# Kernel tuning notes

Measured on AMD Instinct MI355X. Metric: run time of the kernel, lower is better.

Reference implementation:

```python
import jax, jax.numpy as jnp
import numpy as np

N_NODES = 8192
N_EDGES = 65536
D_MODEL = 64
D_INNER = 128
D_STATE = 16
DT_RANK = 4
LAYER_NUM = 3
TAU = 0.01


def _unif(key, shape, fan_out):
    stdv = 1.0 / np.sqrt(fan_out)
    return jax.random.uniform(key, shape, jnp.float32, -stdv, stdv)


def setup_inputs() -> dict:
    key = jax.random.key(0)
    ks = jax.random.split(key, 12)
    x = jax.random.normal(ks[0], (N_NODES, D_MODEL), jnp.float32)
    edge_index = jax.random.randint(ks[1], (2, N_EDGES), 0, N_NODES, jnp.int64)
    in_proj_w = _unif(ks[2], (D_MODEL, 2 * D_INNER), 2 * D_INNER)
    x_proj_w = _unif(ks[3], (D_INNER, DT_RANK + 2 * D_STATE), DT_RANK + 2 * D_STATE)
    dt_proj_w = _unif(ks[4], (DT_RANK, D_INNER), D_INNER)
    out_proj_w = _unif(ks[5], (D_INNER, D_MODEL), D_MODEL)
    A_log = jnp.log(jnp.broadcast_to(jnp.arange(1, D_STATE + 1, dtype=jnp.float32)[None, :], (D_INNER, D_STATE)))
    D = jnp.ones((D_INNER,), jnp.float32)
    in_act_w = _unif(ks[6], (D_INNER, 2), 2)
    in_act_b = _unif(ks[7], (2,), 2)
    out_act_w = _unif(ks[8], (D_INNER, 2), 2)
    out_act_b = _unif(ks[9], (2,), 2)
    return {"x": x, "in_proj_w": in_proj_w, "x_proj_w": x_proj_w, "dt_proj_w": dt_proj_w,
            "A_log": A_log, "D": D, "out_proj_w": out_proj_w,
            "in_act_w": in_act_w, "in_act_b": in_act_b, "out_act_w": out_act_w, "out_act_b": out_act_b,
            "edge_index": edge_index, "layer_num": LAYER_NUM}


def _norm_adj(row, col, w, n_nodes):
    # SparseTensor(...).set_diag() adds diag value 1; symmetric deg^-1/2 renorm
    deg = jax.ops.segment_sum(w, row, num_segments=n_nodes) + 1.0
    dinv = jnp.where(deg > 0, deg ** -0.5, 0.0)
    return dinv[row] * w * dinv[col], dinv * dinv  # off-diag edge weights, diag weights


def _spmm(row, col, ew, dw, x, n_nodes):
    # adj @ x with adj = edges(ew) + diag(dw); x: [N, F]
    return jax.ops.segment_sum(ew[:, None] * x[col], row, num_segments=n_nodes) + dw[:, None] * x


def _gumbel_hard(logits, key, tau):
    g = jax.random.gumbel(key, logits.shape, logits.dtype)
    y = jax.nn.softmax((logits + g) / tau, axis=-1)
    hard = jax.nn.one_hot(jnp.argmax(y, axis=-1), logits.shape[-1], dtype=y.dtype)
    return hard + y - jax.lax.stop_gradient(y)


def reference(x, in_proj_w, x_proj_w, dt_proj_w, A_log, D, out_proj_w,
              in_act_w, in_act_b, out_act_w, out_act_b, edge_index, layer_num):
    n_nodes, d_model = x.shape
    d_inner = dt_proj_w.shape[1]
    n = A_log.shape[1]
    dt_rank = dt_proj_w.shape[0]
    row, col = edge_index[0], edge_index[1]

    xl = jnp.broadcast_to(x[:, None, :], (n_nodes, layer_num, d_model))  # [N,L,d_model]
    x_and_res = xl @ in_proj_w                                           # [N,L,2*d_inner]
    xs, res = jnp.split(x_and_res, 2, axis=-1)
    xs = jax.nn.relu(xs)                                                 # u in scan

    A = -jnp.exp(A_log)                                                  # [d_inner, n]
    x_dbl = xs @ x_proj_w                                                # [N,L,dt_rank+2n]
    delta = jax.nn.softplus(x_dbl[..., :dt_rank] @ dt_proj_w)            # [N,L,d_inner]
    B = x_dbl[..., dt_rank:dt_rank + n]                                  # [N,L,n]
    C = x_dbl[..., dt_rank + n:]                                         # [N,L,n]

    deltaA = jnp.exp(jnp.einsum('bld,dn->bldn', delta, A))               # [N,L,d_inner,n]
    deltaB_u = jnp.einsum('bld,bln->bldn', delta * xs, B)                # [N,L,d_inner,n]

    # initial adjacency: unit-weight edges, sym-normalized with self loops
    ew, dw = _norm_adj(row, col, jnp.ones((row.shape[0],), xs.dtype), n_nodes)
    state = jnp.zeros((n_nodes, d_inner, n), xs.dtype)
    gkey = jax.random.key(42)
    ys = []
    for i in range(layer_num):  # small fixed number of GCN/SSM steps
        state = deltaA[:, i] * state + deltaB_u[:, i]
        y = jnp.einsum('bdn,bn->bd', state, C[:, i])                     # [N,d_inner]
        flat = _spmm(row, col, ew, dw, state.reshape(n_nodes, d_inner * n), n_nodes)
        state = flat.reshape(n_nodes, d_inner, n)
        in_p = _gumbel_hard(y @ in_act_w + in_act_b, jax.random.fold_in(gkey, 2 * i), TAU)
        out_p = _gumbel_hard(y @ out_act_w + out_act_b, jax.random.fold_in(gkey, 2 * i + 1), TAU)
        w = in_p[col, 0] * out_p[row, 0]  # keep_in_prob[v] * keep_out_prob[u]
        ew, dw = _norm_adj(row, col, w, n_nodes)
        ys.append(y)

    y = jnp.stack(ys, axis=1) + xs * D                                   # [N,L,d_inner]
    y = y * jax.nn.relu(res)
    out = y @ out_proj_w                                                 # [N,L,d_model]
    return out[:, -1, :]
```

## Files before the change

### kernel.cpp

```cpp
#include <hip/hip_runtime.h>
#include <cstdint>

#define NN 8192
#define NE 65536
#define G 8
#define CAP 64

typedef _Float16 h4 __attribute__((ext_vector_type(4)));
typedef _Float16 h2 __attribute__((ext_vector_type(2)));

__host__ __device__ inline void tf2x32(uint32_t k0, uint32_t k1,
                                       uint32_t x0, uint32_t x1,
                                       uint32_t& r0, uint32_t& r1) {
  uint32_t ks2 = k0 ^ k1 ^ 0x1BD11BDAu;
  x0 += k0; x1 += k1;
#define TF_ROT(x,d) (((x)<<(d))|((x)>>(32-(d))))
#define TF_R4(ra,rb,rc,rd) \
  x0+=x1; x1=TF_ROT(x1,ra); x1^=x0; \
  x0+=x1; x1=TF_ROT(x1,rb); x1^=x0; \
  x0+=x1; x1=TF_ROT(x1,rc); x1^=x0; \
  x0+=x1; x1=TF_ROT(x1,rd); x1^=x0;
  TF_R4(13,15,26,6)  x0+=k1;  x1+=ks2+1u;
  TF_R4(17,29,16,24) x0+=ks2; x1+=k0+2u;
  TF_R4(13,15,26,6)  x0+=k0;  x1+=k1+3u;
  TF_R4(17,29,16,24) x0+=k1;  x1+=ks2+4u;
  TF_R4(13,15,26,6)  x0+=ks2; x1+=k0+5u;
  r0=x0; r1=x1;
#undef TF_R4
#undef TF_ROT
}

__device__ inline float gumbel32(uint32_t k0, uint32_t k1, uint32_t idx) {
  uint32_t a, b;
  tf2x32(k0, k1, 0u, idx, a, b);
  uint32_t bits = a ^ b;
  float f = __uint_as_float((bits >> 9) | 0x3f800000u) - 1.0f;
  float u = (f > 0.0f) ? f : 1.17549435e-38f;
  return -logf(-logf(u));
}

__global__ void k_zero(int* __restrict__ p, int n) {
  int i = blockIdx.x*blockDim.x + threadIdx.x;
  if (i < n) p[i] = 0;
}

__global__ void k_scatter(const int* __restrict__ ei, int* __restrict__ cnt,
                          int* __restrict__ csr_col) {
  int e = blockIdx.x*blockDim.x + threadIdx.x;
  if (e < NE) {
    int v = ei[e];
    int pos = atomicAdd(&cnt[v], 1);
    if (pos < CAP) csr_col[(v<<6) + pos] = ei[NE + e];
  }
}

__global__ __launch_bounds__(256) void k_nodeprep(
    const float* __restrict__ x, const float* __restrict__ ipw,
    const float* __restrict__ xpw, const float* __restrict__ dtw,
    const float* __restrict__ iaw, const float* __restrict__ iab,
    const float* __restrict__ oaw, const float* __restrict__ oab,
    const float* __restrict__ alog,
    uint32_t ki0, uint32_t ki1, uint32_t ko0, uint32_t ko1,
    float* __restrict__ xs, float* __restrict__ rres,
    float* __restrict__ delta, _Float16* __restrict__ dxh2,
    float* __restrict__ Bm, _Float16* __restrict__ Bh,
    float* __restrict__ Cm,
    float* __restrict__ inp, float* __restrict__ outp,
    float* __restrict__ Amat) {
  __shared__ float sx[G][64];
  __shared__ float sxs[G][128];
  __shared__ float sdbl[G][36];
  __shared__ float sdx[G][128];
  int t = threadIdx.x;
  int b0 = blockIdx.x * G;
  if (blockIdx.x == 0) {
    for (int i = t; i < 2048; i += 256) Amat[i] = -expf(alog[i]);
  }
  for (int i = t; i < G*64; i += 256) sx[i>>6][i&63] = x[b0*64 + i];
  __syncthreads();
  float acc[G];
#pragma unroll
  for (int g = 0; g < G; g++) acc[g] = 0.f;
  for (int k = 0; k < 64; k++) {
    float w = ipw[k*256 + t];
#pragma unroll
    for (int g = 0; g < G; g++) acc[g] += sx[g][k] * w;
  }
  if (t < 128) {
#pragma unroll
    for (int g = 0; g < G; g++) {
      float v = fmaxf(acc[g], 0.f);
      sxs[g][t] = v;
      xs[(size_t)(b0+g)*128 + t] = v;
    }
  } else {
    int j = t - 128;
#pragma unroll
    for (int g = 0; g < G; g++) rres[(size_t)(b0+g)*128 + j] = fmaxf(acc[g], 0.f);
  }
  __syncthreads();
  for (int idx = t; idx < G*36; idx += 256) {
    int g = idx / 36, c = idx % 36;
    float a = 0.f;
    for (int d = 0; d < 128; d++) a += sxs[g][d] * xpw[d*36 + c];
    sdbl[g][c] = a;
    if (c >= 4 && c < 20) {
      Bm[(b0+g)*16 + (c-4)] = a;
      Bh[(b0+g)*16 + (c-4)] = (_Float16)a;
    } else if (c >= 20)    Cm[(b0+g)*16 + (c-20)] = a;
  }
  __syncthreads();
  {
    int d = t & 127, hi = t >> 7;
#pragma unroll
    for (int gg = 0; gg < G/2; gg++) {
      int g = hi*(G/2) + gg;
      int b = b0 + g;
      float dt = sdbl[g][0]*dtw[d]     + sdbl[g][1]*dtw[128+d]
               + sdbl[g][2]*dtw[256+d] + sdbl[g][3]*dtw[384+d];
      float dv = fmaxf(dt, 0.f) + log1pf(expf(-fabsf(dt)));
      delta[(size_t)b*128 + d] = dv;
      sdx[g][d] = dv * sxs[g][d];
    }
  }
  __syncthreads();
  for (int i = t; i < G*64; i += 256) {
    int g = i >> 6, d = i & 63;
    h2 pk;
    pk.x = (_Float16)sdx[g][d];
    pk.y = (_Float16)sdx[g][d + 64];
    ((h2*)(dxh2 + ((size_t)(b0+g) << 7)))[d] = pk;
  }
  int wid = t >> 6, lane = t & 63;
#pragma unroll
  for (int s = 0; s < 2; s++) {
    int g = wid*2 + s;
    int b = b0 + g;
    float da = sdx[g][lane], db = sdx[g][lane + 64];
    float4 pr;
    pr.x = da*iaw[2*lane]   + db*iaw[2*(lane+64)];
    pr.y = da*iaw[2*lane+1] + db*iaw[2*(lane+64)+1];
    pr.z = da*oaw[2*lane]   + db*oaw[2*(lane+64)];
    pr.w = da*oaw[2*lane+1] + db*oaw[2*(lane+64)+1];
    for (int off = 32; off >= 1; off >>= 1) {
      pr.x += __shfl_down(pr.x, off);
      pr.y += __shfl_down(pr.y, off);
      pr.z += __shfl_down(pr.z, off);
      pr.w += __shfl_down(pr.w, off);
    }
    if (lane == 0) {
      float BC = 0.f;
      for (int n = 0; n < 16; n++) BC += sdbl[g][4+n] * sdbl[g][20+n];
      float li0 = BC*pr.x + iab[0], li1 = BC*pr.y + iab[1];
      float lo0 = BC*pr.z + oab[0], lo1 = BC*pr.w + oab[1];
      uint32_t L0 = 2u*(uint32_t)b, L1 = L0 + 1u;
      inp[b]  = (li0 + gumbel32(ki0, ki1, L0) >= li1 + gumbel32(ki0, ki1, L1)) ? 1.0f : 0.0f;
      outp[b] = (lo0 + gumbel32(ko0, ko1, L0) >= lo1 + gumbel32(ko0, ko1, L1)) ? 1.0f : 0.0f;
    }
  }
}

__global__ __launch_bounds__(256) void k_spmm0f(
    const int* __restrict__ cnt, const int* __restrict__ csr_col,
    const float* __restrict__ inp, const float* __restrict__ outp,
    const float* __restrict__ delta, const _Float16* __restrict__ dxh2,
    const float* __restrict__ Bm, const _Float16* __restrict__ Bh,
    const float* __restrict__ Cm, const float* __restrict__ Amat,
    _Float16* __restrict__ s_out, float* __restrict__ dinv1,
    float* __restrict__ y2p) {
  __shared__ int   sc[CAP];
  __shared__ float scoef[CAP];
  __shared__ float sgate[CAP];
  __shared__ float sdegs;
  int v = blockIdx.x, t = threadIdx.x;
  int deg = min(cnt[v], CAP);
  if (t < deg) {
    int c = csr_col[(v<<6) + t];
    sc[t] = c;
    scoef[t] = 1.0f / sqrtf((float)min(cnt[c], CAP) + 1.0f);
    sgate[t] = inp[c];
  }
  __syncthreads();
  if (t < 64) {
    float g = (t < deg) ? sgate[t] : 0.f;
    for (int off = 32; off >= 1; off >>= 1) g += __shfl_down(g, off);
    if (t == 0) sdegs = g;
  }
  int d0 = t >> 2, d1 = d0 + 64, nb = t & 3;
  float dv = 1.0f / sqrtf((float)deg + 1.0f);
  float4 Bv = ((const float4*)(Bm + ((size_t)v << 4)))[nb];
  h2 pkv = ((const h2*)(dxh2 + ((size_t)v << 7)))[d0];
  float dx0 = (float)pkv.x, dx1 = (float)pkv.y;
  float dw = dv * dv;
  float c0 = dw * dx0, c1 = dw * dx1;
  float4 a0 = {c0*Bv.x, c0*Bv.y, c0*Bv.z, c0*Bv.w};
  float4 a1 = {c1*Bv.x, c1*Bv.y, c1*Bv.z, c1*Bv.w};
  for (int j = 0; j < deg; j++) {
    int c = sc[j];
    float coef = dv * scoef[j];
    h2 pk = ((const h2*)(dxh2 + ((size_t)c << 7)))[d0];
    h4 Bp = ((const h4*)(Bh + ((size_t)c << 4)))[nb];
    float e0 = coef * (float)pk.x;
    float e1 = coef * (float)pk.y;
    float bx = (float)Bp.x, by = (float)Bp.y, bz = (float)Bp.z, bw = (float)Bp.w;
    a0.x += e0*bx; a0.y += e0*by; a0.z += e0*bz; a0.w += e0*bw;
    a1.x += e1*bx; a1.y += e1*by; a1.z += e1*bz; a1.w += e1*bw;
  }
  float de0 = delta[v*128 + d0], de1 = delta[v*128 + d1];
  float4 A0 = ((const float4*)(Amat + (d0 << 4)))[nb];
  float4 A1 = ((const float4*)(Amat + (d1 << 4)))[nb];
  float4 E0, E1;
  E0.x = expf(de0*A0.x); E0.y = expf(de0*A0.y); E0.z = expf(de0*A0.z); E0.w = expf(de0*A0.w);
  E1.x = expf(de1*A1.x); E1.y = expf(de1*A1.y); E1.z = expf(de1*A1.z); E1.w = expf(de1*A1.w);
  float4 s0, s1;
  s0.x = E0.x*a0.x + dx0*Bv.x;  s0.y = E0.y*a0.y + dx0*Bv.y;
  s0.z = E0.z*a0.z + dx0*Bv.z;  s0.w = E0.w*a0.w + dx0*Bv.w;
  s1.x = E1.x*a1.x + dx1*Bv.x;  s1.y = E1.y*a1.y + dx1*Bv.y;
  s1.z = E1.z*a1.z + dx1*Bv.z;  s1.w = E1.w*a1.w + dx1*Bv.w;
  if (inp[v] != 0.f) {
    h4* op = (h4*)(s_out + ((size_t)v << 11));
    h4 h0, h1;
    h0.x = (_Float16)s0.x; h0.y = (_Float16)s0.y; h0.z = (_Float16)s0.z; h0.w = (_Float16)s0.w;
    h1.x = (_Float16)s1.x; h1.y = (_Float16)s1.y; h1.z = (_Float16)s1.z; h1.w = (_Float16)s1.w;
    op[t] = h0; op[t + 256] = h1;
  }
  __syncthreads();
  float degs = sdegs;
  float d1v = 1.0f / sqrtf(outp[v]*degs + 1.0f);
  if (t == 0) dinv1[v] = d1v;
  float dw1 = d1v * d1v;
  float4 Cv = ((const float4*)(Cm + ((size_t)v << 4)))[nb];
  float y0p = dw1*(E0.x*s0.x*Cv.x + E0.y*s0.y*Cv.y + E0.z*s0.z*Cv.z + E0.w*s0.w*Cv.w)
            + dx0*(Bv.x*Cv.x + Bv.y*Cv.y + Bv.z*Cv.z + Bv.w*Cv.w);
  float y1p = dw1*(E1.x*s1.x*Cv.x + E1.y*s1.y*Cv.y + E1.z*s1.z*Cv.z + E1.w*s1.w*Cv.w)
            + dx1*(Bv.x*Cv.x + Bv.y*Cv.y + Bv.z*Cv.z + Bv.w*Cv.w);
  y0p += __shfl_xor(y0p, 1); y0p += __shfl_xor(y0p, 2);
  y1p += __shfl_xor(y1p, 1); y1p += __shfl_xor(y1p, 2);
  if (nb == 0) {
    y2p[v*128 + d0] = y0p;
    y2p[v*128 + d1] = y1p;
  }
}

__global__ __launch_bounds__(256) void k_spmm1fo(
    const int* __restrict__ cnt, const int* __restrict__ csr_col,
    const float* __restrict__ dinv1,
    const float* __restrict__ inp, const float* __restrict__ outp,
    const float* __restrict__ delta,
    const float* __restrict__ Cm, const float* __restrict__ Amat,
    const _Float16* __restrict__ s_in, const float* __restrict__ y2p,
    const float* __restrict__ xs, const float* __restrict__ rres,
    const float* __restrict__ Dv, const float* __restrict__ wout,
    float* __restrict__ out) {
  __shared__ int   sc[CAP];
  __shared__ float scoef[CAP];
  __shared__ int   snact;
  __shared__ float ty[128];
  int v = blockIdx.x, t = threadIdx.x;
  if (t == 0) snact = 0;
  __syncthreads();
  int deg = (outp[v] != 0.f) ? min(cnt[v], CAP) : 0;
  if (t < deg) {
    int c = csr_col[(v<<6) + t];
    if (inp[c] != 0.f) {
      int p = atomicAdd(&snact, 1);
      sc[p] = c; scoef[p] = dinv1[c];
    }
  }
  __syncthreads();
  int nact = snact;
  int d0 = t >> 2, d1 = d0 + 64, nb = t & 3;
  float dv = dinv1[v];
  float4 a0 = {0.f,0.f,0.f,0.f}, a1 = {0.f,0.f,0.f,0.f};
  for (int j = 0; j < nact; j++) {
    int c = sc[j];
    float coef = dv * scoef[j];
    const h4* nbp = (const h4*)(s_in + ((size_t)c << 11));
    h4 n0 = nbp[t], n1 = nbp[t + 256];
    a0.x += coef*(float)n0.x; a0.y += coef*(float)n0.y;
    a0.z += coef*(float)n0.z; a0.w += coef*(float)n0.w;
    a1.x += coef*(float)n1.x; a1.y += coef*(float)n1.y;
    a1.z += coef*(float)n1.z; a1.w += coef*(float)n1.w;
  }
  float y0g = 0.f, y1g = 0.f;
  if (nact > 0) {
    float de0 = delta[v*128 + d0], de1 = delta[v*128 + d1];
    float4 A0 = ((const float4*)(Amat + (d0 << 4)))[nb];
    float4 A1 = ((const float4*)(Amat + (d1 << 4)))[nb];
    float4 Cv = ((const float4*)(Cm + ((size_t)v << 4)))[nb];
    y0g = expf(de0*A0.x)*a0.x*Cv.x + expf(de0*A0.y)*a0.y*Cv.y +
          expf(de0*A0.z)*a0.z*Cv.z + expf(de0*A0.w)*a0.w*Cv.w;
    y1g = expf(de1*A1.x)*a1.x*Cv.x + expf(de1*A1.y)*a1.y*Cv.y +
          expf(de1*A1.z)*a1.z*Cv.z + expf(de1*A1.w)*a1.w*Cv.w;
  }
  y0g += __shfl_xor(y0g, 1); y0g += __shfl_xor(y0g, 2);
  y1g += __shfl_xor(y1g, 1); y1g += __shfl_xor(y1g, 2);
  if (nb == 0) {
    float yA = y0g + y2p[v*128 + d0];
    float yB = y1g + y2p[v*128 + d1];
    ty[d0] = (yA + xs[v*128 + d0]*Dv[d0]) * rres[v*128 + d0];
    ty[d1] = (yB + xs[v*128 + d1]*Dv[d1]) * rres[v*128 + d1];
  }
  __syncthreads();
  if (t < 64) {
    float acc = 0.f;
    for (int d = 0; d < 128; d++) acc += ty[d] * wout[d*64 + t];
    out[v*64 + t] = acc;
  }
}

extern "C" void kernel_launch(void* const* d_in, const int* in_sizes, int n_in,
                              void* d_out, int out_size, void* d_ws, size_t ws_size,
                              hipStream_t stream) {
  const float* x    = (const float*)d_in[0];
  const float* ipw  = (const float*)d_in[1];
  const float* xpw  = (const float*)d_in[2];
  const float* dtw  = (const float*)d_in[3];
  const float* alog = (const float*)d_in[4];
  const float* Dv   = (const float*)d_in[5];
  const float* wout = (const float*)d_in[6];
  const float* iaw  = (const float*)d_in[7];
  const float* iab  = (const float*)d_in[8];
  const float* oaw  = (const float*)d_in[9];
  const float* oab  = (const float*)d_in[10];
  const int*   ei   = (const int*)d_in[11];
  (void)in_sizes; (void)n_in; (void)out_size; (void)ws_size;

  float* W = (float*)d_ws;
  size_t o = 0;
  float* xs    = W + o; o += (size_t)NN*128;
  float* rres  = W + o; o += (size_t)NN*128;
  float* delta = W + o; o += (size_t)NN*128;
  float* y2p   = W + o; o += (size_t)NN*128;
  float* Bm    = W + o; o += (size_t)NN*16;
  float* Cm    = W + o; o += (size_t)NN*16;
  float* Amat  = W + o; o += 2048;
  float* dinv1 = W + o; o += NN;
  float* inp   = W + o; o += NN;
  float* outp  = W + o; o += NN;
  _Float16* dxh2 = (_Float16*)(W + o); o += (size_t)NN*64;
  _Float16* Bh   = (_Float16*)(W + o); o += (size_t)NN*8;
  _Float16* stA  = (_Float16*)(W + o); o += (size_t)NN*1024;
  int* cnt     = (int*)(W + o);
  int* csr_col = cnt + NN;

  uint32_t ki0, ki1, ko0, ko1;
  tf2x32(0u, 42u, 0u, 0u, ki0, ki1);
  tf2x32(0u, 42u, 0u, 1u, ko0, ko1);

  k_zero<<<NN/256, 256, 0, stream>>>(cnt, NN);
  k_scatter<<<NE/256, 256, 0, stream>>>(ei, cnt, csr_col);

  k_nodeprep<<<NN/G, 256, 0, stream>>>(x, ipw, xpw, dtw, iaw, iab, oaw, oab,
                                       alog, ki0, ki1, ko0, ko1,
                                       xs, rres, delta, dxh2, Bm, Bh, Cm,
                                       inp, outp, Amat);

  k_spmm0f<<<NN, 256, 0, stream>>>(cnt, csr_col, inp, outp,
                                   delta, dxh2, Bm, Bh, Cm, Amat,
                                   stA, dinv1, y2p);

  k_spmm1fo<<<NN, 256, 0, stream>>>(cnt, csr_col, dinv1, inp, outp,
                                    delta, Cm, Amat, stA, y2p,
                                    xs, rres, Dv, wout, (float*)d_out);
}
```

Measured before the change: 168.7 us.

## Process two nodes per block in SpMM kernels with 8-wide half vectors

Both SpMM kernels now handle two nodes per 256-thread block, with 128 threads per node. Each thread covers 8 state entries using h8 loads and stores instead of 4, so there are fewer shuffle-reduction steps and the grid launches half as many blocks. The output projection is split across all 128 threads with a shared-memory partial sum, replacing the 64-thread loop. The zeroing kernel is replaced by hipMemsetAsync. Per-thread register use and per-neighbor gather width both go up, which could lower occupancy.

```diff
diff --git a/kernel.cpp b/kernel.cpp
--- a/kernel.cpp
+++ b/kernel.cpp
@@ -6,7 +6,7 @@
 #define G 8
 #define CAP 64
 
-typedef _Float16 h4 __attribute__((ext_vector_type(4)));
+typedef _Float16 h8 __attribute__((ext_vector_type(8)));
 typedef _Float16 h2 __attribute__((ext_vector_type(2)));
 
 __host__ __device__ inline void tf2x32(uint32_t k0, uint32_t k1,
@@ -37,11 +37,6 @@
   float f = __uint_as_float((bits >> 9) | 0x3f800000u) - 1.0f;
   float u = (f > 0.0f) ? f : 1.17549435e-38f;
   return -logf(-logf(u));
-}
-
-__global__ void k_zero(int* __restrict__ p, int n) {
-  int i = blockIdx.x*blockDim.x + threadIdx.x;
-  if (i < n) p[i] = 0;
 }
 
 __global__ void k_scatter(const int* __restrict__ ei, int* __restrict__ cnt,
@@ -168,75 +163,96 @@
     const float* __restrict__ Cm, const float* __restrict__ Amat,
     _Float16* __restrict__ s_out, float* __restrict__ dinv1,
     float* __restrict__ y2p) {
-  __shared__ int   sc[CAP];
-  __shared__ float scoef[CAP];
-  __shared__ float sgate[CAP];
-  __shared__ float sdegs;
-  int v = blockIdx.x, t = threadIdx.x;
+  __shared__ int   sc[2][CAP];
+  __shared__ float scoef[2][CAP];
+  __shared__ float sdegs[2];
+  int t = threadIdx.x, half = t >> 7, tid2 = t & 127;
+  int v = (blockIdx.x << 1) + half;
   int deg = min(cnt[v], CAP);
-  if (t < deg) {
-    int c = csr_col[(v<<6) + t];
-    sc[t] = c;
-    scoef[t] = 1.0f / sqrtf((float)min(cnt[c], CAP) + 1.0f);
-    sgate[t] = inp[c];
-  }
-  __syncthreads();
-  if (t < 64) {
-    float g = (t < deg) ? sgate[t] : 0.f;
+  if (tid2 < 64) {
+    float g = 0.f;
+    if (tid2 < deg) {
+      int c = csr_col[(v<<6) + tid2];
+      sc[half][tid2] = c;
+      scoef[half][tid2] = 1.0f / sqrtf((float)min(cnt[c], CAP) + 1.0f);
+      g = inp[c];
+    }
     for (int off = 32; off >= 1; off >>= 1) g += __shfl_down(g, off);
-    if (t == 0) sdegs = g;
-  }
-  int d0 = t >> 2, d1 = d0 + 64, nb = t & 3;
+    if (tid2 == 0) sdegs[half] = g;
+  }
+  __syncthreads();
+  int d0 = tid2 >> 1, d1 = d0 + 64, nq = tid2 & 1;
   float dv = 1.0f / sqrtf((float)deg + 1.0f);
-  float4 Bv = ((const float4*)(Bm + ((size_t)v << 4)))[nb];
+  const float4* BmV = (const float4*)(Bm + ((size_t)v << 4));
+  float4 Bv0 = BmV[nq*2], Bv1 = BmV[nq*2+1];
   h2 pkv = ((const h2*)(dxh2 + ((size_t)v << 7)))[d0];
   float dx0 = (float)pkv.x, dx1 = (float)pkv.y;
   float dw = dv * dv;
   float c0 = dw * dx0, c1 = dw * dx1;
-  float4 a0 = {c0*Bv.x, c0*Bv.y, c0*Bv.z, c0*Bv.w};
-  float4 a1 = {c1*Bv.x, c1*Bv.y, c1*Bv.z, c1*Bv.w};
+  float4 a0l = {c0*Bv0.x, c0*Bv0.y, c0*Bv0.z, c0*Bv0.w};
+  float4 a0h = {c0*Bv1.x, c0*Bv1.y, c0*Bv1.z, c0*Bv1.w};
+  float4 a1l = {c1*Bv0.x, c1*Bv0.y, c1*Bv0.z, c1*Bv0.w};
+  float4 a1h = {c1*Bv1.x, c1*Bv1.y, c1*Bv1.z, c1*Bv1.w};
   for (int j = 0; j < deg; j++) {
-    int c = sc[j];
-    float coef = dv * scoef[j];
+    int c = sc[half][j];
+    float coef = dv * scoef[half][j];
     h2 pk = ((const h2*)(dxh2 + ((size_t)c << 7)))[d0];
-    h4 Bp = ((const h4*)(Bh + ((size_t)c << 4)))[nb];
+    h8 Bp = ((const h8*)(Bh + ((size_t)c << 4)))[nq];
     float e0 = coef * (float)pk.x;
     float e1 = coef * (float)pk.y;
-    float bx = (float)Bp.x, by = (float)Bp.y, bz = (float)Bp.z, bw = (float)Bp.w;
-    a0.x += e0*bx; a0.y += e0*by; a0.z += e0*bz; a0.w += e0*bw;
-    a1.x += e1*bx; a1.y += e1*by; a1.z += e1*bz; a1.w += e1*bw;
+    float b0f = (float)Bp[0], b1f = (float)Bp[1], b2f = (float)Bp[2], b3f = (float)Bp[3];
+    float b4f = (float)Bp[4], b5f = (float)Bp[5], b6f = (float)Bp[6], b7f = (float)Bp[7];
+    a0l.x += e0*b0f; a0l.y += e0*b1f; a0l.z += e0*b2f; a0l.w += e0*b3f;
+    a0h.x += e0*b4f; a0h.y += e0*b5f; a0h.z += e0*b6f; a0h.w += e0*b7f;
+    a1l.x += e1*b0f; a1l.y += e1*b1f; a1l.z += e1*b2f; a1l.w += e1*b3f;
+    a1h.x += e1*b4f; a1h.y += e1*b5f; a1h.z += e1*b6f; a1h.w += e1*b7f;
   }
   float de0 = delta[v*128 + d0], de1 = delta[v*128 + d1];
-  float4 A0 = ((const float4*)(Amat + (d0 << 4)))[nb];
-  float4 A1 = ((const float4*)(Amat + (d1 << 4)))[nb];
-  float4 E0, E1;
-  E0.x = expf(de0*A0.x); E0.y = expf(de0*A0.y); E0.z = expf(de0*A0.z); E0.w = expf(de0*A0.w);
-  E1.x = expf(de1*A1.x); E1.y = expf(de1*A1.y); E1.z = expf(de1*A1.z); E1.w = expf(de1*A1.w);
-  float4 s0, s1;
-  s0.x = E0.x*a0.x + dx0*Bv.x;  s0.y = E0.y*a0.y + dx0*Bv.y;
-  s0.z = E0.z*a0.z + dx0*Bv.z;  s0.w = E0.w*a0.w + dx0*Bv.w;
-  s1.x = E1.x*a1.x + dx1*Bv.x;  s1.y = E1.y*a1.y + dx1*Bv.y;
-  s1.z = E1.z*a1.z + dx1*Bv.z;  s1.w = E1.w*a1.w + dx1*Bv.w;
+  const float4* A0p = (const float4*)(Amat + (d0 << 4));
+  const float4* A1p = (const float4*)(Amat + (d1 << 4));
+  float4 A00 = A0p[nq*2], A01 = A0p[nq*2+1];
+  float4 A10 = A1p[nq*2], A11 = A1p[nq*2+1];
+  float4 E0l, E0h, E1l, E1h;
+  E0l.x = expf(de0*A00.x); E0l.y = expf(de0*A00.y); E0l.z = expf(de0*A00.z); E0l.w = expf(de0*A00.w);
+  E0h.x = expf(de0*A01.x); E0h.y = expf(de0*A01.y); E0h.z = expf(de0*A01.z); E0h.w = expf(de0*A01.w);
+  E1l.x = expf(de1*A10.x); E1l.y = expf(de1*A10.y); E1l.z = expf(de1*A10.z); E1l.w = expf(de1*A10.w);
+  E1h.x = expf(de1*A11.x); E1h.y = expf(de1*A11.y); E1h.z = expf(de1*A11.z); E1h.w = expf(de1*A11.w);
+  float4 s0l, s0h, s1l, s1h;
+  s0l.x = E0l.x*a0l.x + dx0*Bv0.x; s0l.y = E0l.y*a0l.y + dx0*Bv0.y;
+  s0l.z = E0l.z*a0l.z + dx0*Bv0.z; s0l.w = E0l.w*a0l.w + dx0*Bv0.w;
+  s0h.x = E0h.x*a0h.x + dx0*Bv1.x; s0h.y = E0h.y*a0h.y + dx0*Bv1.y;
+  s0h.z = E0h.z*a0h.z + dx0*Bv1.z; s0h.w = E0h.w*a0h.w + dx0*Bv1.w;
+  s1l.x = E1l.x*a1l.x + dx1*Bv0.x; s1l.y = E1l.y*a1l.y + dx1*Bv0.y;
+  s1l.z = E1l.z*a1l.z + dx1*Bv0.z; s1l.w = E1l.w*a1l.w + dx1*Bv0.w;
+  s1h.x = E1h.x*a1h.x + dx1*Bv1.x; s1h.y = E1h.y*a1h.y + dx1*Bv1.y;
+  s1h.z = E1h.z*a1h.z + dx1*Bv1.z; s1h.w = E1h.w*a1h.w + dx1*Bv1.w;
   if (inp[v] != 0.f) {
-    h4* op = (h4*)(s_out + ((size_t)v << 11));
-    h4 h0, h1;
-    h0.x = (_Float16)s0.x; h0.y = (_Float16)s0.y; h0.z = (_Float16)s0.z; h0.w = (_Float16)s0.w;
-    h1.x = (_Float16)s1.x; h1.y = (_Float16)s1.y; h1.z = (_Float16)s1.z; h1.w = (_Float16)s1.w;
-    op[t] = h0; op[t + 256] = h1;
-  }
-  __syncthreads();
-  float degs = sdegs;
+    h8* op = (h8*)(s_out + ((size_t)v << 11));
+    h8 p0, p1;
+    p0[0]=(_Float16)s0l.x; p0[1]=(_Float16)s0l.y; p0[2]=(_Float16)s0l.z; p0[3]=(_Float16)s0l.w;
+    p0[4]=(_Float16)s0h.x; p0[5]=(_Float16)s0h.y; p0[6]=(_Float16)s0h.z; p0[7]=(_Float16)s0h.w;
+    p1[0]=(_Float16)s1l.x; p1[1]=(_Float16)s1l.y; p1[2]=(_Float16)s1l.z; p1[3]=(_Float16)s1l.w;
+    p1[4]=(_Float16)s1h.x; p1[5]=(_Float16)s1h.y; p1[6]=(_Float16)s1h.z; p1[7]=(_Float16)s1h.w;
+    op[d0*2 + nq] = p0;
+    op[d0*2 + 128 + nq] = p1;
+  }
+  float degs = sdegs[half];
   float d1v = 1.0f / sqrtf(outp[v]*degs + 1.0f);
-  if (t == 0) dinv1[v] = d1v;
+  if (tid2 == 0) dinv1[v] = d1v;
   float dw1 = d1v * d1v;
-  float4 Cv = ((const float4*)(Cm + ((size_t)v << 4)))[nb];
-  float y0p = dw1*(E0.x*s0.x*Cv.x + E0.y*s0.y*Cv.y + E0.z*s0.z*Cv.z + E0.w*s0.w*Cv.w)
-            + dx0*(Bv.x*Cv.x + Bv.y*Cv.y + Bv.z*Cv.z + Bv.w*Cv.w);
-  float y1p = dw1*(E1.x*s1.x*Cv.x + E1.y*s1.y*Cv.y + E1.z*s1.z*Cv.z + E1.w*s1.w*Cv.w)
-            + dx1*(Bv.x*Cv.x + Bv.y*Cv.y + Bv.z*Cv.z + Bv.w*Cv.w);
-  y0p += __shfl_xor(y0p, 1); y0p += __shfl_xor(y0p, 2);
-  y1p += __shfl_xor(y1p, 1); y1p += __shfl_xor(y1p, 2);
-  if (nb == 0) {
+  const float4* CmV = (const float4*)(Cm + ((size_t)v << 4));
+  float4 Cv0 = CmV[nq*2], Cv1 = CmV[nq*2+1];
+  float BvC = Bv0.x*Cv0.x + Bv0.y*Cv0.y + Bv0.z*Cv0.z + Bv0.w*Cv0.w
+            + Bv1.x*Cv1.x + Bv1.y*Cv1.y + Bv1.z*Cv1.z + Bv1.w*Cv1.w;
+  float y0p = dw1*(E0l.x*s0l.x*Cv0.x + E0l.y*s0l.y*Cv0.y + E0l.z*s0l.z*Cv0.z + E0l.w*s0l.w*Cv0.w
+                 + E0h.x*s0h.x*Cv1.x + E0h.y*s0h.y*Cv1.y + E0h.z*s0h.z*Cv1.z + E0h.w*s0h.w*Cv1.w)
+            + dx0*BvC;
+  float y1p = dw1*(E1l.x*s1l.x*Cv0.x + E1l.y*s1l.y*Cv0.y + E1l.z*s1l.z*Cv0.z + E1l.w*s1l.w*Cv0.w
+                 + E1h.x*s1h.x*Cv1.x + E1h.y*s1h.y*Cv1.y + E1h.z*s1h.z*Cv1.z + E1h.w*s1h.w*Cv1.w)
+            + dx1*BvC;
+  y0p += __shfl_xor(y0p, 1);
+  y1p += __shfl_xor(y1p, 1);
+  if (nq == 0) {
     y2p[v*128 + d0] = y0p;
     y2p[v*128 + d1] = y1p;
   }
@@ -252,61 +268,78 @@
     const float* __restrict__ xs, const float* __restrict__ rres,
     const float* __restrict__ Dv, const float* __restrict__ wout,
     float* __restrict__ out) {
-  __shared__ int   sc[CAP];
-  __shared__ float scoef[CAP];
-  __shared__ int   snact;
-  __shared__ float ty[128];
-  int v = blockIdx.x, t = threadIdx.x;
-  if (t == 0) snact = 0;
-  __syncthreads();
-  int deg = (outp[v] != 0.f) ? min(cnt[v], CAP) : 0;
-  if (t < deg) {
-    int c = csr_col[(v<<6) + t];
-    if (inp[c] != 0.f) {
-      int p = atomicAdd(&snact, 1);
-      sc[p] = c; scoef[p] = dinv1[c];
-    }
-  }
-  __syncthreads();
-  int nact = snact;
-  int d0 = t >> 2, d1 = d0 + 64, nb = t & 3;
+  __shared__ int   sc[2][CAP];
+  __shared__ float scoef[2][CAP];
+  __shared__ int   snact[2];
+  __shared__ float ty[2][128];
+  __shared__ float sproj[2][64];
+  int t = threadIdx.x, half = t >> 7, tid2 = t & 127;
+  int v = (blockIdx.x << 1) + half;
+  if (tid2 == 0) snact[half] = 0;
+  if (tid2 < 64) {
+    int deg = (outp[v] != 0.f) ? min(cnt[v], CAP) : 0;
+    if (tid2 < deg) {
+      int c = csr_col[(v<<6) + tid2];
+      if (inp[c] != 0.f) {
+        int p = atomicAdd(&snact[half], 1);
+        sc[half][p] = c; scoef[half][p] = dinv1[c];
+      }
+    }
+  }
+  __syncthreads();
+  int nact = snact[half];
+  int d0 = tid2 >> 1, d1 = d0 + 64, nq = tid2 & 1;
   float dv = dinv1[v];
-  float4 a0 = {0.f,0.f,0.f,0.f}, a1 = {0.f,0.f,0.f,0.f};
+  float4 a0l = {0.f,0.f,0.f,0.f}, a0h = {0.f,0.f,0.f,0.f};
+  float4 a1l = {0.f,0.f,0.f,0.f}, a1h = {0.f,0.f,0.f,0.f};
   for (int j = 0; j < nact; j++) {
-    int c = sc[j];
-    float coef = dv * scoef[j];
-    const h4* nbp = (const h4*)(s_in + ((size_t)c << 11));
-    h4 n0 = nbp[t], n1 = nbp[t + 256];
-    a0.x += coef*(float)n0.x; a0.y += coef*(float)n0.y;
-    a0.z += coef*(float)n0.z; a0.w += coef*(float)n0.w;
-    a1.x += coef*(float)n1.x; a1.y += coef*(float)n1.y;
-    a1.z += coef*(float)n1.z; a1.w += coef*(float)n1.w;
+    int c = sc[half][j];
+    float coef = dv * scoef[half][j];
+    const h8* rp = (const h8*)(s_in + ((size_t)c << 11));
+    h8 n0 = rp[d0*2 + nq], n1 = rp[d0*2 + 128 + nq];
+    a0l.x += coef*(float)n0[0]; a0l.y += coef*(float)n0[1];
+    a0l.z += coef*(float)n0[2]; a0l.w += coef*(float)n0[3];
+    a0h.x += coef*(float)n0[4]; a0h.y += coef*(float)n0[5];
+    a0h.z += coef*(float)n0[6]; a0h.w += coef*(float)n0[7];
+    a1l.x += coef*(float)n1[0]; a1l.y += coef*(float)n1[1];
+    a1l.z += coef*(float)n1[2]; a1l.w += coef*(float)n1[3];
+    a1h.x += coef*(float)n1[4]; a1h.y += coef*(float)n1[5];
+    a1h.z += coef*(float)n1[6]; a1h.w += coef*(float)n1[7];
   }
   float y0g = 0.f, y1g = 0.f;
   if (nact > 0) {
     float de0 = delta[v*128 + d0], de1 = delta[v*128 + d1];
-    float4 A0 = ((const float4*)(Amat + (d0 << 4)))[nb];
-    float4 A1 = ((const float4*)(Amat + (d1 << 4)))[nb];
-    float4 Cv = ((const float4*)(Cm + ((size_t)v << 4)))[nb];
-    y0g = expf(de0*A0.x)*a0.x*Cv.x + expf(de0*A0.y)*a0.y*Cv.y +
-          expf(de0*A0.z)*a0.z*Cv.z + expf(de0*A0.w)*a0.w*Cv.w;
-    y1g = expf(de1*A1.x)*a1.x*Cv.x + expf(de1*A1.y)*a1.y*Cv.y +
-          expf(de1*A1.z)*a1.z*Cv.z + expf(de1*A1.w)*a1.w*Cv.w;
-  }
-  y0g += __shfl_xor(y0g, 1); y0g += __shfl_xor(y0g, 2);
-  y1g += __shfl_xor(y1g, 1); y1g += __shfl_xor(y1g, 2);
-  if (nb == 0) {
+    const float4* A0p = (const float4*)(Amat + (d0 << 4));
+    const float4* A1p = (const float4*)(Amat + (d1 << 4));
+    float4 A00 = A0p[nq*2], A01 = A0p[nq*2+1];
+    float4 A10 = A1p[nq*2], A11 = A1p[nq*2+1];
+    const float4* CmV = (const float4*)(Cm + ((size_t)v << 4));
+    float4 Cv0 = CmV[nq*2], Cv1 = CmV[nq*2+1];
+    y0g = expf(de0*A00.x)*a0l.x*Cv0.x + expf(de0*A00.y)*a0l.y*Cv0.y
+        + expf(de0*A00.z)*a0l.z*Cv0.z + expf(de0*A00.w)*a0l.w*Cv0.w
+        + expf(de0*A01.x)*a0h.x*Cv1.x + expf(de0*A01.y)*a0h.y*Cv1.y
+        + expf(de0*A01.z)*a0h.z*Cv1.z + expf(de0*A01.w)*a0h.w*Cv1.w;
+    y1g = expf(de1*A10.x)*a1l.x*Cv0.x + expf(de1*A10.y)*a1l.y*Cv0.y
+        + expf(de1*A10.z)*a1l.z*Cv0.z + expf(de1*A10.w)*a1l.w*Cv0.w
+        + expf(de1*A11.x)*a1h.x*Cv1.x + expf(de1*A11.y)*a1h.y*Cv1.y
+        + expf(de1*A11.z)*a1h.z*Cv1.z + expf(de1*A11.w)*a1h.w*Cv1.w;
+  }
+  y0g += __shfl_xor(y0g, 1);
+  y1g += __shfl_xor(y1g, 1);
+  if (nq == 0) {
     float yA = y0g + y2p[v*128 + d0];
     float yB = y1g + y2p[v*128 + d1];
-    ty[d0] = (yA + xs[v*128 + d0]*Dv[d0]) * rres[v*128 + d0];
-    ty[d1] = (yB + xs[v*128 + d1]*Dv[d1]) * rres[v*128 + d1];
-  }
-  __syncthreads();
-  if (t < 64) {
-    float acc = 0.f;
-    for (int d = 0; d < 128; d++) acc += ty[d] * wout[d*64 + t];
-    out[v*64 + t] = acc;
-  }
+    ty[half][d0] = (yA + xs[v*128 + d0]*Dv[d0]) * rres[v*128 + d0];
+    ty[half][d1] = (yB + xs[v*128 + d1]*Dv[d1]) * rres[v*128 + d1];
+  }
+  __syncthreads();
+  int oc = tid2 & 63, ks = tid2 >> 6;
+  const float* typ = ty[half];
+  float acc = 0.f;
+  for (int d = ks*64; d < ks*64 + 64; d++) acc += typ[d] * wout[d*64 + oc];
+  if (ks == 1) sproj[half][oc] = acc;
+  __syncthreads();
+  if (ks == 0) out[v*64 + oc] = acc + sproj[half][oc];
 }
 
 extern "C" void kernel_launch(void* const* d_in, const int* in_sizes, int n_in,
@@ -348,7 +381,7 @@
   tf2x32(0u, 42u, 0u, 0u, ki0, ki1);
   tf2x32(0u, 42u, 0u, 1u, ko0, ko1);
 
-  k_zero<<<NN/256, 256, 0, stream>>>(cnt, NN);
+  hipMemsetAsync(cnt, 0, NN*sizeof(int), stream);
   k_scatter<<<NE/256, 256, 0, stream>>>(ei, cnt, csr_col);
 
   k_nodeprep<<<NN/G, 256, 0, stream>>>(x, ipw, xpw, dtw, iaw, iab, oaw, oab,
@@ -356,11 +389,11 @@
                                        xs, rres, delta, dxh2, Bm, Bh, Cm,
                                        inp, outp, Amat);
 
-  k_spmm0f<<<NN, 256, 0, stream>>>(cnt, csr_col, inp, outp,
-                                   delta, dxh2, Bm, Bh, Cm, Amat,
-                                   stA, dinv1, y2p);
-
-  k_spmm1fo<<<NN, 256, 0, stream>>>(cnt, csr_col, dinv1, inp, outp,
-                                    delta, Cm, Amat, stA, y2p,
-                                    xs, rres, Dv, wout, (float*)d_out);
-}
+  k_spmm0f<<<NN/2, 256, 0, stream>>>(cnt, csr_col, inp, outp,
+                                     delta, dxh2, Bm, Bh, Cm, Amat,
+                                     stA, dinv1, y2p);
+
+  k_spmm1fo<<<NN/2, 256, 0, stream>>>(cnt, csr_col, dinv1, inp, outp,
+                                      delta, Cm, Amat, stA, y2p,
+                                      xs, rres, Dv, wout, (float*)d_out);
+}
```

After: 168.8 us. About the same (+0.1%).
